# Performance work log

Measured on AMD Instinct MI355X. Metric: run time of the kernel, lower is better.

## Reference

```python
import jax, jax.numpy as jnp
import numpy as np
import math

V, L, D, S, F, H, B = 32000, 6, 1024, 2048, 4096, 16, 2
DK = D // H
EPS = 1e-5


def _pos_encoding(max_len, d_model):
    pos = np.arange(max_len)[:, None].astype(np.float32)
    freq = np.exp(np.arange(0, d_model, 2).astype(np.float32) * -(math.log(10000.0) / d_model))
    pe = np.zeros((max_len, d_model), dtype=np.float32)
    pe[:, 0::2] = np.sin(pos * freq)
    pe[:, 1::2] = np.cos(pos * freq)
    return jnp.asarray(pe)


def setup_inputs() -> dict:
    key = jax.random.key(0)
    ks = jax.random.split(key, 16)
    n = lambda k, shape: (jax.random.normal(k, shape, dtype=jnp.float32) * 0.02)
    return {
        "tokens": jax.random.randint(ks[0], (B, S), 0, V, dtype=jnp.int32),
        "emb": n(ks[1], (V, D)),
        "Wq": n(ks[2], (L, D, D)), "bq": jnp.zeros((L, D)),
        "Wk": n(ks[3], (L, D, D)), "bk": jnp.zeros((L, D)),
        "Wv": n(ks[4], (L, D, D)), "bv": jnp.zeros((L, D)),
        "Wo": n(ks[5], (L, D, D)), "bo": jnp.zeros((L, D)),
        "W1": n(ks[6], (L, D, F)), "b1": jnp.zeros((L, F)),
        "W2": n(ks[7], (L, F, D)), "b2": jnp.zeros((L, D)),
        "g1": jnp.ones((L, D)), "be1": jnp.zeros((L, D)),
        "g2": jnp.ones((L, D)), "be2": jnp.zeros((L, D)),
    }


def _layernorm(x, g, b):
    mu = jnp.mean(x, axis=-1, keepdims=True)
    var = jnp.var(x, axis=-1, keepdims=True)
    return (x - mu) * jax.lax.rsqrt(var + EPS) * g + b


def _encoder(tokens, emb, Wq, bq, Wk, bk, Wv, bv, Wo, bo, W1, b1, W2, b2, g1, be1, g2, be2):
    pe = _pos_encoding(S, D)
    x = emb[tokens] * jnp.float32(math.sqrt(D)) + pe  # [B,S,D]

    def layer(x, p):
        wq, bq_, wk, bk_, wv, bv_, wo, bo_, w1, b1_, w2, b2_, g1_, be1_, g2_, be2_ = p
        q = (x @ wq + bq_).reshape(B, S, H, DK)
        k = (x @ wk + bk_).reshape(B, S, H, DK)
        v = (x @ wv + bv_).reshape(B, S, H, DK)
        scores = jnp.einsum("bqhd,bkhd->bhqk", q, k) / jnp.float32(math.sqrt(DK))
        attn = jax.nn.softmax(scores, axis=-1)
        out = jnp.einsum("bhqk,bkhd->bqhd", attn, v).reshape(B, S, D)
        out = out @ wo + bo_
        x = _layernorm(x + out, g1_, be1_)
        ff = jax.nn.relu(x @ w1 + b1_) @ w2 + b2_
        x = _layernorm(x + ff, g2_, be2_)
        return x, None

    params = (Wq, bq, Wk, bk, Wv, bv, Wo, bo, W1, b1, W2, b2, g1, be1, g2, be2)
    x, _ = jax.lax.scan(layer, x, params)
    return x


def reference(tokens, emb, Wq, bq, Wk, bk, Wv, bv, Wo, bo, W1, b1, W2, b2, g1, be1, g2, be2):
    return _encoder(tokens, emb, Wq, bq, Wk, bk, Wv, bv, Wo, bo, W1, b1, W2, b2, g1, be1, g2, be2)
```

## Files before the change

kernel.cpp:

```cpp
#include <hip/hip_runtime.h>
#include <hip/hip_bf16.h>

#define DEV static __device__ __forceinline__

typedef __attribute__((ext_vector_type(8))) short bf16x8;
typedef __attribute__((ext_vector_type(4))) float f32x4;
typedef __attribute__((ext_vector_type(4))) unsigned short u16x4;
typedef __attribute__((ext_vector_type(4))) unsigned int u32x4;

constexpr int Lc = 6, Dc = 1024, Sc = 2048, Fc = 4096, Hc = 16, Bc = 2;
constexpr int Mc = Bc * Sc;
constexpr int QKVN = 3 * Dc;
constexpr float QSCALE = 0.18033688011112042f;

DEV float bf2f(unsigned short u) {
  unsigned int x = ((unsigned int)u) << 16; float f;
  __builtin_memcpy(&f, &x, 4); return f;
}
DEV unsigned short f2bf(float f) {
  unsigned int x; __builtin_memcpy(&x, &f, 4);
  x += 0x7fffu + ((x >> 16) & 1u);
  return (unsigned short)(x >> 16);
}
DEV unsigned int cvt_pk_bf16(float lo, float hi) {
  unsigned int r;
  asm("v_cvt_pk_bf16_f32 %0, %1, %2" : "=v"(r) : "v"(lo), "v"(hi));
  return r;
}

typedef __attribute__((address_space(1))) unsigned int* gas_t;
typedef __attribute__((address_space(3))) unsigned int* las_t;
DEV void gload16(const void* g, void* l) {
  __builtin_amdgcn_global_load_lds((gas_t)g, (las_t)l, 16, 0, 0);
}

__global__ __launch_bounds__(256) void transpose_f2b(
    const float* __restrict__ W, unsigned short* __restrict__ Wt,
    int Kd, int Nd, float scale)
{
  __shared__ float tile[32][33];
  const int n0 = blockIdx.x * 32, k0 = blockIdx.y * 32;
  const int tx = threadIdx.x & 31, ty = threadIdx.x >> 5;
#pragma unroll
  for (int i = 0; i < 4; ++i) {
    int k = ty + i * 8;
    tile[k][tx] = W[(size_t)(k0 + k) * Nd + n0 + tx];
  }
  __syncthreads();
#pragma unroll
  for (int i = 0; i < 4; ++i) {
    int n = ty + i * 8;
    Wt[(size_t)(n0 + n) * Kd + k0 + tx] = f2bf(tile[tx][n] * scale);
  }
}

DEV int vperm(int k) {
  return ((k >> 5) << 5) + (((k >> 2) & 3) << 3) + (((k >> 4) & 1) << 2) + (k & 3);
}
__global__ __launch_bounds__(256) void transpose_v(
    const unsigned short* __restrict__ QKV, unsigned short* __restrict__ Vt)
{
  __shared__ unsigned short tile[32][33];
  const int s0 = blockIdx.x * 32, c0 = blockIdx.y * 32, b = blockIdx.z;
  const int tx = threadIdx.x & 31, ty = threadIdx.x >> 5;
  const unsigned short* src = QKV + ((size_t)b * Sc) * QKVN + 2 * Dc;
#pragma unroll
  for (int i = 0; i < 4; ++i) {
    int s = ty + i * 8;
    tile[s][tx] = src[(size_t)(s0 + s) * QKVN + c0 + tx];
  }
  __syncthreads();
  unsigned short* dst = Vt + (size_t)b * Dc * Sc;
  const int s = s0 + tx;
  const int sp = (s & ~63) + vperm(s & 63);
#pragma unroll
  for (int i = 0; i < 4; ++i) {
    int c = ty + i * 8;
    dst[(size_t)(c0 + c) * Sc + sp] = tile[tx][c];
  }
}

__global__ __launch_bounds__(256) void pack_bias(
    const float* __restrict__ bq, const float* __restrict__ bk,
    const float* __restrict__ bv, float* __restrict__ out)
{
  int i = blockIdx.x * 256 + threadIdx.x;
  out[i] = (i < Dc) ? bq[i] * QSCALE : (i < 2 * Dc ? bk[i - Dc] : bv[i - 2 * Dc]);
}

__global__ __launch_bounds__(256) void embed_kernel(
    const int* __restrict__ tokens, const float* __restrict__ emb,
    float* __restrict__ xf, unsigned short* __restrict__ xb)
{
  const int bs = blockIdx.x;
  const int s = bs & (Sc - 1);
  const int tok = tokens[bs];
  const int d0 = threadIdx.x * 4;
  f32x4 e4 = *(const f32x4*)(emb + (size_t)tok * Dc + d0);
  f32x4 vf; u16x4 vb;
#pragma unroll
  for (int j = 0; j < 4; ++j) {
    int d = d0 + j;
    float e = e4[j] * 32.0f;
    float fr = expf((float)(d & ~1) * (-9.210340371976184f / 1024.0f));
    float arg = (float)s * fr;
    float pe = (d & 1) ? cosf(arg) : sinf(arg);
    float v = e + pe;
    vf[j] = v; vb[j] = f2bf(v);
  }
  *(f32x4*)(xf + (size_t)bs * Dc + d0) = vf;
  *(u16x4*)(xb + (size_t)bs * Dc + d0) = vb;
}

DEV void gemm_core(const unsigned short* A, const unsigned short* Bt,
                   unsigned short* As, unsigned short* Bs,
                   f32x4 (*acc)[4], int mTile, int nTile,
                   int Kstride, int k0, int k1, int t)
{
  const int lane = t & 63;
  const int w = t >> 6;
  const int wm = w >> 1, wn = w & 1;
  for (int kt = k0; kt < k1; kt += 64) {
    __syncthreads();
#pragma unroll
    for (int i = 0; i < 4; ++i) {
      int idx = i * 256 + t;
      int row = idx >> 3;
      int sl = (idx & 7) ^ (row & 7);
      gload16(A + (size_t)(mTile + row) * Kstride + kt + sl * 8, &As[idx * 8]);
      gload16(Bt + (size_t)(nTile + row) * Kstride + kt + sl * 8, &Bs[idx * 8]);
    }
    __syncthreads();
#pragma unroll
    for (int ks = 0; ks < 2; ++ks) {
      const int kb = ks * 64 + ((lane >> 4) << 4);
      bf16x8 a[4], b[4];
#pragma unroll
      for (int mi = 0; mi < 4; ++mi) {
        int r = wm * 64 + mi * 16 + (lane & 15);
        a[mi] = *(const bf16x8*)((const char*)As + r * 128 + (kb ^ ((r & 7) << 4)));
      }
#pragma unroll
      for (int ni = 0; ni < 4; ++ni) {
        int r = wn * 64 + ni * 16 + (lane & 15);
        b[ni] = *(const bf16x8*)((const char*)Bs + r * 128 + (kb ^ ((r & 7) << 4)));
      }
#pragma unroll
      for (int mi = 0; mi < 4; ++mi)
#pragma unroll
        for (int ni = 0; ni < 4; ++ni)
          acc[mi][ni] = __builtin_amdgcn_mfma_f32_16x16x32_bf16(
              a[mi], b[ni], acc[mi][ni], 0, 0, 0);
    }
  }
}

__global__ __launch_bounds__(256) void gemm128(
    const unsigned short* __restrict__ A, const unsigned short* __restrict__ Bt,
    const float* __restrict__ bias, unsigned short* __restrict__ outB,
    int gx, int Ndim, int Kdim, int relu)
{
  __shared__ alignas(16) unsigned short As[128 * 64];
  __shared__ alignas(16) unsigned short Bs[128 * 64];
  const int t = threadIdx.x;
  const int lane = t & 63;
  const int w = t >> 6;
  const int wm = w >> 1, wn = w & 1;
  const int nwg = gridDim.x, flat = blockIdx.x;
  const int swz = (flat & 7) * (nwg >> 3) + (flat >> 3);
  const int mTile = (swz / gx) * 128;
  const int nTile = (swz % gx) * 128;

  f32x4 acc[4][4] = {};
  gemm_core(A, Bt, As, Bs, acc, mTile, nTile, Kdim, 0, Kdim, t);

#pragma unroll
  for (int mi = 0; mi < 4; ++mi) {
#pragma unroll
    for (int ni = 0; ni < 4; ++ni) {
      const int c = nTile + wn * 64 + ni * 16 + (lane & 15);
      const float bvv = bias[c];
#pragma unroll
      for (int j = 0; j < 4; ++j) {
        const int r = mTile + wm * 64 + mi * 16 + ((lane >> 4) << 2) + j;
        float v = acc[mi][ni][j] + bvv;
        if (relu) v = fmaxf(v, 0.0f);
        outB[(size_t)r * Ndim + c] = f2bf(v);
      }
    }
  }
}

template<int SPLIT>
__global__ __launch_bounds__(256) void gemm_sk(
    const unsigned short* __restrict__ A, const unsigned short* __restrict__ Bt,
    float* __restrict__ part, int gx, int gy, int Ndim, int Ktot)
{
  __shared__ alignas(16) unsigned short As[128 * 64];
  __shared__ alignas(16) unsigned short Bs[128 * 64];
  const int t = threadIdx.x;
  const int lane = t & 63;
  const int w = t >> 6;
  const int wm = w >> 1, wn = w & 1;
  const int nwg = gridDim.x, flat = blockIdx.x;
  const int swz = (flat & 7) * (nwg >> 3) + (flat >> 3);
  const int nTile = (swz % gx) * 128;
  const int mTile = ((swz / gx) % gy) * 128;
  const int z = swz / (gx * gy);
  const int Kseg = Ktot / SPLIT;

  f32x4 acc[4][4] = {};
  gemm_core(A, Bt, As, Bs, acc, mTile, nTile, Ktot, z * Kseg, (z + 1) * Kseg, t);

  float* po = part + (size_t)z * Mc * Ndim;
#pragma unroll
  for (int mi = 0; mi < 4; ++mi)
#pragma unroll
    for (int ni = 0; ni < 4; ++ni) {
      const int c = nTile + wn * 64 + ni * 16 + (lane & 15);
#pragma unroll
      for (int j = 0; j < 4; ++j) {
        const int r = mTile + wm * 64 + mi * 16 + ((lane >> 4) << 2) + j;
        po[(size_t)r * Ndim + c] = acc[mi][ni][j];
      }
    }
}

__global__ __launch_bounds__(256) void attn128(
    const unsigned short* __restrict__ QKV, const unsigned short* __restrict__ Vt,
    unsigned short* __restrict__ O)
{
  __shared__ alignas(16) unsigned short Qs[128 * 64];
  __shared__ alignas(16) unsigned short Ks[2][64 * 64];
  __shared__ alignas(16) unsigned short Vs[2][64 * 64];

  const int t = threadIdx.x;
  const int lane = t & 63, w = t >> 6;
  const int g = lane >> 4, li = lane & 15;
  const int flat = blockIdx.x;
  const int idx = ((flat & 7) << 6) | (flat >> 3);
  const int qb = idx & 15, bh = idx >> 4;
  const int b = bh >> 4, h = bh & 15;

  const size_t qbase  = ((size_t)(b * Sc + qb * 128)) * QKVN + h * 64;
  const size_t kbase0 = ((size_t)b * Sc) * QKVN + Dc + h * 64;
  const size_t vbase0 = ((size_t)(b * Dc + h * 64)) * Sc;

#pragma unroll
  for (int i = 0; i < 4; ++i) {
    int idx2 = i * 256 + t, row = idx2 >> 3, sl = (idx2 & 7) ^ (row & 7);
    gload16(QKV + qbase + (size_t)row * QKVN + sl * 8, &Qs[idx2 * 8]);
  }
  const unsigned short* kg[2];
  const unsigned short* vg[2];
  int loff[2];
#pragma unroll
  for (int i = 0; i < 2; ++i) {
    int idx2 = i * 256 + t, row = idx2 >> 3, sl = (idx2 & 7) ^ (row & 7);
    kg[i] = QKV + kbase0 + (size_t)row * QKVN + sl * 8;
    vg[i] = Vt + vbase0 + (size_t)row * Sc + sl * 8;
    loff[i] = idx2 * 8;
  }
  gload16(kg[0], &Ks[0][loff[0]]); gload16(kg[1], &Ks[0][loff[1]]);
  gload16(vg[0], &Vs[0][loff[0]]); gload16(vg[1], &Vs[0][loff[1]]);
  kg[0] += 64 * QKVN; kg[1] += 64 * QKVN;
  vg[0] += 64;        vg[1] += 64;
  __syncthreads();

  bf16x8 qf[2][2];
#pragma unroll
  for (int qi = 0; qi < 2; ++qi) {
    const int rq = w * 32 + qi * 16 + li;
#pragma unroll
    for (int ks = 0; ks < 2; ++ks) {
      const int kb = ks * 64 + (g << 4);
      qf[qi][ks] = *(const bf16x8*)((const char*)Qs + rq * 128 + (kb ^ ((rq & 7) << 4)));
    }
  }
  bf16x8 ones;
#pragma unroll
  for (int e = 0; e < 8; ++e) ones[e] = (short)0x3F80;

  f32x4 acc_o[2][4] = {};
  f32x4 acc_l[2] = {};
  int cur = 0;

  for (int kc = 0; kc < Sc; kc += 64) {
    if (kc + 64 < Sc) {
      const int nxt = cur ^ 1;
      gload16(kg[0], &Ks[nxt][loff[0]]); gload16(kg[1], &Ks[nxt][loff[1]]);
      gload16(vg[0], &Vs[nxt][loff[0]]); gload16(vg[1], &Vs[nxt][loff[1]]);
      kg[0] += 64 * QKVN; kg[1] += 64 * QKVN;
      vg[0] += 64;        vg[1] += 64;
    }

    f32x4 accs[2][4] = {};
#pragma unroll
    for (int ks = 0; ks < 2; ++ks) {
      const int kb = ks * 64 + (g << 4);
#pragma unroll
      for (int ni = 0; ni < 4; ++ni) {
        int rk = ni * 16 + li;
        bf16x8 ak = *(const bf16x8*)((const char*)Ks[cur] + rk * 128 + (kb ^ ((rk & 7) << 4)));
        accs[0][ni] = __builtin_amdgcn_mfma_f32_16x16x32_bf16(ak, qf[0][ks], accs[0][ni], 0, 0, 0);
        accs[1][ni] = __builtin_amdgcn_mfma_f32_16x16x32_bf16(ak, qf[1][ks], accs[1][ni], 0, 0, 0);
      }
    }

    unsigned int pk[2][4][2];
#pragma unroll
    for (int qi = 0; qi < 2; ++qi)
#pragma unroll
      for (int ni = 0; ni < 4; ++ni) {
        float p0 = exp2f(accs[qi][ni][0]);
        float p1 = exp2f(accs[qi][ni][1]);
        float p2 = exp2f(accs[qi][ni][2]);
        float p3 = exp2f(accs[qi][ni][3]);
        pk[qi][ni][0] = cvt_pk_bf16(p0, p1);
        pk[qi][ni][1] = cvt_pk_bf16(p2, p3);
      }

#pragma unroll
    for (int ks = 0; ks < 2; ++ks) {
      bf16x8 ap[2];
#pragma unroll
      for (int qi = 0; qi < 2; ++qi) {
        u32x4 av = {pk[qi][2 * ks][0], pk[qi][2 * ks][1],
                    pk[qi][2 * ks + 1][0], pk[qi][2 * ks + 1][1]};
        ap[qi] = __builtin_bit_cast(bf16x8, av);
        acc_l[qi] = __builtin_amdgcn_mfma_f32_16x16x32_bf16(ap[qi], ones, acc_l[qi], 0, 0, 0);
      }
      const int kb = ks * 64 + (g << 4);
#pragma unroll
      for (int ni = 0; ni < 4; ++ni) {
        int rd = ni * 16 + li;
        bf16x8 bv = *(const bf16x8*)((const char*)Vs[cur] + rd * 128 + (kb ^ ((rd & 7) << 4)));
        acc_o[0][ni] = __builtin_amdgcn_mfma_f32_16x16x32_bf16(ap[0], bv, acc_o[0][ni], 0, 0, 0);
        acc_o[1][ni] = __builtin_amdgcn_mfma_f32_16x16x32_bf16(ap[1], bv, acc_o[1][ni], 0, 0, 0);
      }
    }

    __syncthreads();
    cur ^= 1;
  }

  const size_t obase = ((size_t)(b * Sc + qb * 128)) * Dc + h * 64;
#pragma unroll
  for (int qi = 0; qi < 2; ++qi) {
    float denom[4];
#pragma unroll
    for (int j = 0; j < 4; ++j) denom[j] = 1.0f / acc_l[qi][j];
#pragma unroll
    for (int ni = 0; ni < 4; ++ni)
#pragma unroll
      for (int j = 0; j < 4; ++j) {
        int q = w * 32 + qi * 16 + g * 4 + j;
        O[obase + (size_t)q * Dc + ni * 16 + li] = f2bf(acc_o[qi][ni][j] * denom[j]);
      }
  }
}

template<int SPLIT>
__global__ __launch_bounds__(256) void reduce_ln(
    const float* __restrict__ part, const float* __restrict__ bias,
    const float* __restrict__ res, const float* __restrict__ g,
    const float* __restrict__ be, float* __restrict__ xf_out,
    unsigned short* __restrict__ xb_out)
{
  const int row = blockIdx.x, t = threadIdx.x;
  const size_t off = (size_t)row * Dc + t * 4;
  f32x4 v = *(const f32x4*)(res + off);
  v += *(const f32x4*)(bias + t * 4);
#pragma unroll
  for (int s = 0; s < SPLIT; ++s)
    v += *(const f32x4*)(part + (size_t)s * Mc * Dc + off);

  float sm = v[0] + v[1] + v[2] + v[3];
  float q = v[0]*v[0] + v[1]*v[1] + v[2]*v[2] + v[3]*v[3];
#pragma unroll
  for (int o = 32; o; o >>= 1) {
    sm += __shfl_down(sm, o);
    q += __shfl_down(q, o);
  }
  __shared__ float rs_[4], rq_[4];
  const int lane = t & 63, w = t >> 6;
  if (lane == 0) { rs_[w] = sm; rq_[w] = q; }
  __syncthreads();
  sm = rs_[0] + rs_[1] + rs_[2] + rs_[3];
  q = rq_[0] + rq_[1] + rq_[2] + rq_[3];
  const float mu = sm * (1.0f / 1024.0f);
  const float var = q * (1.0f / 1024.0f) - mu * mu;
  const float rstd = rsqrtf(var + 1e-5f);
  f32x4 vg = *(const f32x4*)(g + t * 4);
  f32x4 vb = *(const f32x4*)(be + t * 4);
  f32x4 o; u16x4 ob;
#pragma unroll
  for (int j = 0; j < 4; ++j) {
    float val = (v[j] - mu) * rstd * vg[j] + vb[j];
    o[j] = val; ob[j] = f2bf(val);
  }
  *(f32x4*)(xf_out + off) = o;
  *(u16x4*)(xb_out + off) = ob;
}

extern "C" void kernel_launch(void* const* d_in, const int* in_sizes, int n_in,
                              void* d_out, int out_size, void* d_ws, size_t ws_size,
                              hipStream_t stream)
{
  (void)in_sizes; (void)n_in; (void)out_size; (void)ws_size;
  const int*   tokens = (const int*)d_in[0];
  const float* emb = (const float*)d_in[1];
  const float* Wq = (const float*)d_in[2];
  const float* bq = (const float*)d_in[3];
  const float* Wk = (const float*)d_in[4];
  const float* bk = (const float*)d_in[5];
  const float* Wv = (const float*)d_in[6];
  const float* bv = (const float*)d_in[7];
  const float* Wo = (const float*)d_in[8];
  const float* bo = (const float*)d_in[9];
  const float* W1 = (const float*)d_in[10];
  const float* b1 = (const float*)d_in[11];
  const float* W2 = (const float*)d_in[12];
  const float* b2 = (const float*)d_in[13];
  const float* g1 = (const float*)d_in[14];
  const float* be1 = (const float*)d_in[15];
  const float* g2 = (const float*)d_in[16];
  const float* be2 = (const float*)d_in[17];

  char* p = (char*)d_ws;
  auto take = [&](size_t bytes) { char* q = p; p += bytes; return q; };
  unsigned short* Wqkvt = (unsigned short*)take((size_t)3 * Dc * Dc * 2);
  unsigned short* Wot = (unsigned short*)take((size_t)Dc * Dc * 2);
  unsigned short* W1t = (unsigned short*)take((size_t)Dc * Fc * 2);
  unsigned short* W2t = (unsigned short*)take((size_t)Fc * Dc * 2);
  float*          bqkv = (float*)take((size_t)QKVN * 4);
  float*          xf  = (float*)take((size_t)Mc * Dc * 4);
  unsigned short* xb  = (unsigned short*)take((size_t)Mc * Dc * 2);
  unsigned short* QKVb = (unsigned short*)take((size_t)Mc * QKVN * 2);
  unsigned short* Vtb = (unsigned short*)take((size_t)Bc * Dc * Sc * 2);
  unsigned short* Ob  = (unsigned short*)take((size_t)Mc * Dc * 2);
  unsigned short* ff1 = (unsigned short*)take((size_t)Mc * Fc * 2);
  float* part = (float*)QKVb;

  dim3 blk(256);
  embed_kernel<<<dim3(Mc), blk, 0, stream>>>(tokens, emb, xf, xb);

  for (int l = 0; l < Lc; ++l) {
    const size_t owD = (size_t)l * Dc * Dc;
    const size_t owF = (size_t)l * Dc * Fc;
    const int ob = l * Dc;
    transpose_f2b<<<dim3(Dc / 32, Dc / 32), blk, 0, stream>>>(Wq + owD, Wqkvt, Dc, Dc, QSCALE);
    transpose_f2b<<<dim3(Dc / 32, Dc / 32), blk, 0, stream>>>(Wk + owD, Wqkvt + (size_t)Dc * Dc, Dc, Dc, 1.0f);
    transpose_f2b<<<dim3(Dc / 32, Dc / 32), blk, 0, stream>>>(Wv + owD, Wqkvt + (size_t)2 * Dc * Dc, Dc, Dc, 1.0f);
    transpose_f2b<<<dim3(Dc / 32, Dc / 32), blk, 0, stream>>>(Wo + owD, Wot, Dc, Dc, 1.0f);
    transpose_f2b<<<dim3(Fc / 32, Dc / 32), blk, 0, stream>>>(W1 + owF, W1t, Dc, Fc, 1.0f);
    transpose_f2b<<<dim3(Dc / 32, Fc / 32), blk, 0, stream>>>(W2 + owF, W2t, Fc, Dc, 1.0f);
    pack_bias<<<dim3(QKVN / 256), blk, 0, stream>>>(bq + ob, bk + ob, bv + ob, bqkv);

    gemm128<<<dim3((QKVN / 128) * (Mc / 128)), blk, 0, stream>>>(
        xb, Wqkvt, bqkv, QKVb, QKVN / 128, QKVN, Dc, 0);
    transpose_v<<<dim3(Sc / 32, Dc / 32, Bc), blk, 0, stream>>>(QKVb, Vtb);
    attn128<<<dim3(512), blk, 0, stream>>>(QKVb, Vtb, Ob);

    gemm_sk<2><<<dim3((Dc / 128) * (Mc / 128) * 2), blk, 0, stream>>>(
        Ob, Wot, part, Dc / 128, Mc / 128, Dc, Dc);
    reduce_ln<2><<<dim3(Mc), blk, 0, stream>>>(
        part, bo + ob, xf, g1 + ob, be1 + ob, xf, xb);

    gemm128<<<dim3((Fc / 128) * (Mc / 128)), blk, 0, stream>>>(
        xb, W1t, b1 + l * Fc, ff1, Fc / 128, Fc, Dc, 1);

    gemm_sk<2><<<dim3((Dc / 128) * (Mc / 128) * 2), blk, 0, stream>>>(
        ff1, W2t, part, Dc / 128, Mc / 128, Dc, Fc);
    reduce_ln<2><<<dim3(Mc), blk, 0, stream>>>(
        part, b2 + ob, xf, g2 + ob, be2 + ob,
        (l == Lc - 1) ? (float*)d_out : xf, xb);
  }
}
```

Before: 1.602 ms.

## Replace 128x128 GEMM with double-buffered 256x256 pipelined GEMM for QKV and FFN1

Introduces a 512-thread 256x256-tile GEMM kernel whose LDS is double-buffered. Loads for the next K-step are issued in four phases interleaved with MFMA work, using explicit vmcnt waits, barriers and setprio, and the kernel replaces gemm128 for the QKV and first FFN projections. Larger tiles raise arithmetic intensity and cut global traffic, and the overlap hides load latency. In exchange it uses 128KB of LDS per block, which limits occupancy, and it launches fewer blocks (192 and 256), which may underfill the CUs.

```diff
diff --git a/kernel.cpp b/kernel.cpp
--- a/kernel.cpp
+++ b/kernel.cpp
@@ -112,6 +112,130 @@
   *(u16x4*)(xb + (size_t)bs * Dc + d0) = vb;
 }
 
+__global__ __launch_bounds__(512) void gemm256(
+    const unsigned short* __restrict__ A, const unsigned short* __restrict__ Bt,
+    const float* __restrict__ bias, unsigned short* __restrict__ outB,
+    int gx, int Ndim, int Kdim, int relu)
+{
+  __shared__ alignas(16) unsigned short As[2][256 * 64];
+  __shared__ alignas(16) unsigned short Bs[2][256 * 64];
+  const int t = threadIdx.x;
+  const int lane = t & 63, w = t >> 6;
+  const int wm = w >> 2, wn = w & 3;
+  const int g = lane >> 4, li = lane & 15;
+  const int nwg = gridDim.x, flat = blockIdx.x;
+  const int swz = (flat & 7) * (nwg >> 3) + (flat >> 3);
+  const int mTile = (swz / gx) * 256;
+  const int nTile = (swz % gx) * 256;
+
+  const int trow = t >> 3, tslot = t & 7;
+  const int asl = tslot ^ (trow & 7);
+  int aoff[4];
+#pragma unroll
+  for (int q = 0; q < 4; ++q) {
+    int R = (trow < 32) ? (q * 32 + trow) : (96 + q * 32 + trow);
+    aoff[q] = (mTile + R) * Kdim + asl * 8;
+  }
+  int boff[4], bld[4];
+#pragma unroll
+  for (int k2 = 0; k2 < 4; ++k2) {
+    int idx = k2 * 512 + t;
+    int br = idx >> 3;
+    int bs = (idx & 7) ^ (br & 7);
+    boff[k2] = (nTile + br) * Kdim + bs * 8;
+    bld[k2] = idx * 8;
+  }
+
+  auto stB = [&](int nb, int kt, int ph) {
+    gload16(Bt + boff[ph * 2 + 0] + kt, &Bs[nb][bld[ph * 2 + 0]]);
+    gload16(Bt + boff[ph * 2 + 1] + kt, &Bs[nb][bld[ph * 2 + 1]]);
+  };
+  auto stA = [&](int nb, int kt, int ph) {
+    gload16(A + aoff[ph * 2 + 0] + kt, &As[nb][(ph * 2 + 0) * 4096 + t * 8]);
+    gload16(A + aoff[ph * 2 + 1] + kt, &As[nb][(ph * 2 + 1) * 4096 + t * 8]);
+  };
+
+  f32x4 acc[8][4] = {};
+
+  stB(0, 0, 0); stB(0, 0, 1); stA(0, 0, 0); stA(0, 0, 1);
+  asm volatile("s_waitcnt vmcnt(0)" ::: "memory");
+  __builtin_amdgcn_s_barrier();
+
+  const int nT = Kdim >> 6;
+  int cur = 0;
+  for (int tt = 0; tt < nT; ++tt) {
+    const char* Ac = (const char*)As[cur];
+    const char* Bc = (const char*)Bs[cur];
+    const int nb = cur ^ 1;
+    const int ktn = (tt + 1) << 6;
+    const bool more = tt + 1 < nT;
+
+    bf16x8 bfr[4][2];
+#pragma unroll
+    for (int ni = 0; ni < 4; ++ni) {
+      const int rn = wn * 64 + ni * 16 + li;
+#pragma unroll
+      for (int ks = 0; ks < 2; ++ks) {
+        const int kb = ks * 64 + (g << 4);
+        bfr[ni][ks] = *(const bf16x8*)(Bc + rn * 128 + (kb ^ ((rn & 7) << 4)));
+      }
+    }
+
+#pragma unroll
+    for (int ph = 0; ph < 4; ++ph) {
+      bf16x8 afr[2][2];
+#pragma unroll
+      for (int mi2 = 0; mi2 < 2; ++mi2) {
+        const int rr = wm * 32 + mi2 * 16 + li;
+#pragma unroll
+        for (int ks = 0; ks < 2; ++ks) {
+          const int kb = ks * 64 + (g << 4);
+          afr[mi2][ks] = *(const bf16x8*)(Ac + ph * 8192 + rr * 128 + (kb ^ ((rr & 7) << 4)));
+        }
+      }
+      if (more) {
+        if (ph == 0)      stB(nb, ktn, 0);
+        else if (ph == 1) stB(nb, ktn, 1);
+        else if (ph == 2) stA(nb, ktn, 0);
+        else              stA(nb, ktn, 1);
+      }
+      __builtin_amdgcn_s_barrier();
+      __builtin_amdgcn_s_setprio(1);
+#pragma unroll
+      for (int mi2 = 0; mi2 < 2; ++mi2)
+#pragma unroll
+        for (int ni = 0; ni < 4; ++ni)
+#pragma unroll
+          for (int ks = 0; ks < 2; ++ks)
+            acc[ph * 2 + mi2][ni] = __builtin_amdgcn_mfma_f32_16x16x32_bf16(
+                afr[mi2][ks], bfr[ni][ks], acc[ph * 2 + mi2][ni], 0, 0, 0);
+      __builtin_amdgcn_s_setprio(0);
+      if (ph == 0)      asm volatile("s_waitcnt vmcnt(4)" ::: "memory");
+      else if (ph == 1) asm volatile("s_waitcnt vmcnt(5)" ::: "memory");
+      else if (ph == 2) asm volatile("s_waitcnt vmcnt(6)" ::: "memory");
+      else              asm volatile("s_waitcnt vmcnt(3)" ::: "memory");
+      __builtin_amdgcn_s_barrier();
+    }
+    cur ^= 1;
+  }
+
+#pragma unroll
+  for (int mi = 0; mi < 8; ++mi) {
+#pragma unroll
+    for (int ni = 0; ni < 4; ++ni) {
+      const int c = nTile + wn * 64 + ni * 16 + li;
+      const float bvv = bias[c];
+#pragma unroll
+      for (int j = 0; j < 4; ++j) {
+        const int r = mTile + wm * 128 + mi * 16 + g * 4 + j;
+        float v = acc[mi][ni][j] + bvv;
+        if (relu) v = fmaxf(v, 0.0f);
+        outB[(size_t)r * Ndim + c] = f2bf(v);
+      }
+    }
+  }
+}
+
 DEV void gemm_core(const unsigned short* A, const unsigned short* Bt,
                    unsigned short* As, unsigned short* Bs,
                    f32x4 (*acc)[4], int mTile, int nTile,
@@ -151,42 +275,6 @@
         for (int ni = 0; ni < 4; ++ni)
           acc[mi][ni] = __builtin_amdgcn_mfma_f32_16x16x32_bf16(
               a[mi], b[ni], acc[mi][ni], 0, 0, 0);
-    }
-  }
-}
-
-__global__ __launch_bounds__(256) void gemm128(
-    const unsigned short* __restrict__ A, const unsigned short* __restrict__ Bt,
-    const float* __restrict__ bias, unsigned short* __restrict__ outB,
-    int gx, int Ndim, int Kdim, int relu)
-{
-  __shared__ alignas(16) unsigned short As[128 * 64];
-  __shared__ alignas(16) unsigned short Bs[128 * 64];
-  const int t = threadIdx.x;
-  const int lane = t & 63;
-  const int w = t >> 6;
-  const int wm = w >> 1, wn = w & 1;
-  const int nwg = gridDim.x, flat = blockIdx.x;
-  const int swz = (flat & 7) * (nwg >> 3) + (flat >> 3);
-  const int mTile = (swz / gx) * 128;
-  const int nTile = (swz % gx) * 128;
-
-  f32x4 acc[4][4] = {};
-  gemm_core(A, Bt, As, Bs, acc, mTile, nTile, Kdim, 0, Kdim, t);
-
-#pragma unroll
-  for (int mi = 0; mi < 4; ++mi) {
-#pragma unroll
-    for (int ni = 0; ni < 4; ++ni) {
-      const int c = nTile + wn * 64 + ni * 16 + (lane & 15);
-      const float bvv = bias[c];
-#pragma unroll
-      for (int j = 0; j < 4; ++j) {
-        const int r = mTile + wm * 64 + mi * 16 + ((lane >> 4) << 2) + j;
-        float v = acc[mi][ni][j] + bvv;
-        if (relu) v = fmaxf(v, 0.0f);
-        outB[(size_t)r * Ndim + c] = f2bf(v);
-      }
     }
   }
 }
@@ -457,8 +545,8 @@
     transpose_f2b<<<dim3(Dc / 32, Fc / 32), blk, 0, stream>>>(W2 + owF, W2t, Fc, Dc, 1.0f);
     pack_bias<<<dim3(QKVN / 256), blk, 0, stream>>>(bq + ob, bk + ob, bv + ob, bqkv);
 
-    gemm128<<<dim3((QKVN / 128) * (Mc / 128)), blk, 0, stream>>>(
-        xb, Wqkvt, bqkv, QKVb, QKVN / 128, QKVN, Dc, 0);
+    gemm256<<<dim3((Mc / 256) * (QKVN / 256)), dim3(512), 0, stream>>>(
+        xb, Wqkvt, bqkv, QKVb, QKVN / 256, QKVN, Dc, 0);
     transpose_v<<<dim3(Sc / 32, Dc / 32, Bc), blk, 0, stream>>>(QKVb, Vtb);
     attn128<<<dim3(512), blk, 0, stream>>>(QKVb, Vtb, Ob);
 
@@ -467,8 +555,8 @@
     reduce_ln<2><<<dim3(Mc), blk, 0, stream>>>(
         part, bo + ob, xf, g1 + ob, be1 + ob, xf, xb);
 
-    gemm128<<<dim3((Fc / 128) * (Mc / 128)), blk, 0, stream>>>(
-        xb, W1t, b1 + l * Fc, ff1, Fc / 128, Fc, Dc, 1);
+    gemm256<<<dim3((Mc / 256) * (Fc / 256)), dim3(512), 0, stream>>>(
+        xb, W1t, b1 + l * Fc, ff1, Fc / 256, Fc, Dc, 1);
 
     gemm_sk<2><<<dim3((Dc / 128) * (Mc / 128) * 2), blk, 0, stream>>>(
         ff1, W2t, part, Dc / 128, Mc / 128, Dc, Fc);
```

Measured after the change: 1.480 ms. 7.6% less time.
